# Performance work log

Hardware: AMD Instinct MI355X
Metric: run time of the kernel (lower is better)

## Reference

```python
import jax, jax.numpy as jnp
import numpy as np

HIDDEN = 1024

def setup_inputs() -> dict:
    key = jax.random.key(0)
    ks = jax.random.split(key, 7)
    B, S, H = 4, 2048, HIDDEN
    scale = 1.0 / np.sqrt(H)
    x = jax.random.normal(ks[0], (B, S, H), dtype=jnp.float32)
    Wq = jax.random.normal(ks[1], (H, H), dtype=jnp.float32) * scale
    Wk = jax.random.normal(ks[2], (H, H), dtype=jnp.float32) * scale
    Wv = jax.random.normal(ks[3], (H, H), dtype=jnp.float32) * scale
    bq = jax.random.normal(ks[4], (H,), dtype=jnp.float32) * 0.01
    bk = jax.random.normal(ks[5], (H,), dtype=jnp.float32) * 0.01
    bv = jax.random.normal(ks[6], (H,), dtype=jnp.float32) * 0.01
    return {"x": x, "Wq": Wq, "bq": bq, "Wk": Wk, "bk": bk, "Wv": Wv, "bv": bv}

def reference(x, Wq, bq, Wk, bk, Wv, bv):
    H = x.shape[-1]
    # Linear layers: y = x @ W^T + b (torch convention)
    Q = jnp.einsum('bsh,oh->bso', x, Wq) + bq
    K = jnp.einsum('bsh,oh->bso', x, Wk) + bk
    V = jnp.einsum('bsh,oh->bso', x, Wv) + bv
    # full O(S^2) score matrix, scaled by sqrt(hidden_dim) as in the source
    scores = jnp.einsum('bqh,bkh->bqk', Q, K) / jnp.sqrt(jnp.asarray(H, x.dtype))
    weights = jax.nn.softmax(scores, axis=-1)  # dropout is identity at inference
    out = jnp.einsum('bqk,bkh->bqh', weights, V)
    return out
```

## Files before the change

kernel.cpp:

```cpp
#include <hip/hip_runtime.h>
#include <hip/hip_bf16.h>

typedef __attribute__((ext_vector_type(8))) short bf16x8;
typedef __attribute__((ext_vector_type(4))) float f32x4;
typedef unsigned short u16;
typedef unsigned int u32;


__device__ __forceinline__ u16 f2bf(float f) {
  union { float f; u32 u; } v; v.f = f;
  u32 r = v.u + 0x7FFFu + ((v.u >> 16) & 1u);
  return (u16)(r >> 16);
}

__device__ __forceinline__ void gload_lds16(const u16* g, u16* l) {
  __builtin_amdgcn_global_load_lds(
      (const __attribute__((address_space(1))) u32*)(const void*)g,
      (__attribute__((address_space(3))) u32*)(void*)l, 16, 0, 0);
}


__global__ __launch_bounds__(256) void cvt_all(const float* __restrict__ x,
                                               const float* __restrict__ wq,
                                               const float* __restrict__ wk,
                                               const float* __restrict__ wv,
                                               u16* __restrict__ xb,
                                               u16* __restrict__ wcat) {
  const int bid = blockIdx.x;
  const float* src; u16* dst; size_t base;
  if (bid < 4096) { src = x; dst = xb; base = (size_t)bid * 2048; }
  else {
    int w = bid - 4096, s = w >> 9;
    src = (s == 0) ? wq : ((s == 1) ? wk : wv);
    dst = wcat + (size_t)s * 1048576;
    base = (size_t)(w & 511) * 2048;
  }
  size_t i = base + (size_t)threadIdx.x * 8;
  const float4* p = (const float4*)(src + i);
  float4 a = p[0], b = p[1];
  union { u16 u[8]; uint4 v; } r;
  r.u[0] = f2bf(a.x); r.u[1] = f2bf(a.y); r.u[2] = f2bf(a.z); r.u[3] = f2bf(a.w);
  r.u[4] = f2bf(b.x); r.u[5] = f2bf(b.y); r.u[6] = f2bf(b.z); r.u[7] = f2bf(b.w);
  *(uint4*)(dst + i) = r.v;
}


template<int MODE, int BM, int BN>
__global__ __launch_bounds__(512, 2) void gemm_pipe(
    const u16* __restrict__ A, const u16* __restrict__ B,
    const float* __restrict__ b0, const float* __restrict__ b1,
    const float* __restrict__ b2,
    void* __restrict__ o0, void* __restrict__ o1, void* __restrict__ o2,
    float* __restrict__ lsum, int lda, int ldb, int nkt,
    long Abat, long Bbat) {
  extern __shared__ u16 lds[];
  constexpr int NMT = BM / 32;
  constexpr int ANL = BM / 64;
  constexpr int BNL = BN / 64;
  constexpr int ASZ = BM * 64, BSZ = BN * 64;

  const int tid = threadIdx.x;
  const int lane = tid & 63, wv = tid >> 6;
  const int lr = lane & 15, lg = lane >> 4;
  const int wm = wv >> 2, wn = wv & 3;
  const int bm = blockIdx.x * BM, bn = blockIdx.y * BN;
  const int bz = blockIdx.z;

  const u16* Ab; const u16* Bb;
  if constexpr (MODE == 3) {
    Ab = A;
    Bb = B + (size_t)Bbat * (bm >> 11);
  } else {
    Ab = A + (size_t)Abat * bz;
    Bb = B + (size_t)Bbat * bz;
  }

  f32x4 acc[NMT][4];
#pragma unroll
  for (int i = 0; i < NMT; ++i)
#pragma unroll
    for (int j = 0; j < 4; ++j) acc[i][j] = (f32x4)0.0f;

  auto stage = [&](int kt, int buf) {
    u16* As = lds + buf * (ASZ + BSZ);
    u16* Bs = As + ASZ;
    const int k0 = kt * 64;
#pragma unroll
    for (int j = 0; j < ANL; ++j) {
      int id = j * 512 + tid, row = id >> 3, c = id & 7, cg = c ^ (row & 7);
      gload_lds16(Ab + (size_t)(bm + row) * lda + k0 + cg * 8, As + id * 8);
    }
#pragma unroll
    for (int j = 0; j < BNL; ++j) {
      int id = j * 512 + tid, row = id >> 3, c = id & 7, cg = c ^ (row & 7);
      gload_lds16(Bb + (size_t)(bn + row) * ldb + k0 + cg * 8, Bs + id * 8);
    }
  };

  stage(0, 0);
  __syncthreads();

  for (int kt = 0; kt < nkt; ++kt) {
    if (kt + 1 < nkt) stage(kt + 1, (kt + 1) & 1);
    __builtin_amdgcn_sched_barrier(0);
    const u16* As = lds + (kt & 1) * (ASZ + BSZ);
    const u16* Bs = As + ASZ;
#pragma unroll
    for (int kk = 0; kk < 2; ++kk) {
      bf16x8 a[NMT], b[4];
#pragma unroll
      for (int mt = 0; mt < NMT; ++mt) {
        int row = wm * (BM / 2) + mt * 16 + lr;
        int kc = (kk * 4 + lg) ^ (row & 7);
        a[mt] = *(const bf16x8*)(As + row * 64 + kc * 8);
      }
#pragma unroll
      for (int nt = 0; nt < 4; ++nt) {
        int row = wn * 64 + nt * 16 + lr;
        int kc = (kk * 4 + lg) ^ (row & 7);
        b[nt] = *(const bf16x8*)(Bs + row * 64 + kc * 8);
      }
#pragma unroll
      for (int mt = 0; mt < NMT; ++mt)
#pragma unroll
        for (int nt = 0; nt < 4; ++nt)
          acc[mt][nt] = __builtin_amdgcn_mfma_f32_16x16x32_bf16(a[mt], b[nt], acc[mt][nt], 0, 0, 0);
    }
    __syncthreads();
  }

  if constexpr (MODE == 0) {
    const int sel = bn >> 10;
    const float* bp = (sel == 0) ? b0 : ((sel == 1) ? b1 : b2);
#pragma unroll
    for (int nt = 0; nt < 4; ++nt) {
      int gcol = bn + wn * 64 + nt * 16 + lr;
      int col = gcol & 1023;
      float bv = bp[col];
#pragma unroll
      for (int mt = 0; mt < NMT; ++mt) {
        int grow0 = bm + wm * (BM / 2) + mt * 16 + lg * 4;
        if (sel < 2) {
          u16* o = sel ? (u16*)o1 : (u16*)o0;
#pragma unroll
          for (int r = 0; r < 4; ++r)
            o[(size_t)(grow0 + r) * 1024 + col] = f2bf(acc[mt][nt][r] + bv);
        } else {
          u16* o = (u16*)o2;
          int batch = grow0 >> 11, s = grow0 & 2047;
          union { u16 u[4]; uint2 v; } pk;
#pragma unroll
          for (int r = 0; r < 4; ++r) pk.u[r] = f2bf(acc[mt][nt][r] + bv);
          *(uint2*)(o + (((size_t)(batch * 1024 + col)) << 11) + s) = pk.v;
        }
      }
    }
  } else if constexpr (MODE == 2) {
    u16* P = (u16*)o0 + (size_t)2048 * 2048 * bz;
    float psum[NMT][4];
#pragma unroll
    for (int mt = 0; mt < NMT; ++mt)
#pragma unroll
      for (int r = 0; r < 4; ++r) psum[mt][r] = 0.0f;
#pragma unroll
    for (int nt = 0; nt < 4; ++nt) {
      int gcol = bn + wn * 64 + nt * 16 + lr;
#pragma unroll
      for (int mt = 0; mt < NMT; ++mt) {
        int grow0 = bm + wm * (BM / 2) + mt * 16 + lg * 4;
#pragma unroll
        for (int r = 0; r < 4; ++r) {
          float e = __expf(acc[mt][nt][r] * 0.03125f);
          P[(size_t)(grow0 + r) * 2048 + gcol] = f2bf(e);
          psum[mt][r] += e;
        }
      }
    }
#pragma unroll
    for (int mt = 0; mt < NMT; ++mt)
#pragma unroll
      for (int r = 0; r < 4; ++r) {
#pragma unroll
        for (int off = 1; off < 16; off <<= 1)
          psum[mt][r] += __shfl_xor(psum[mt][r], off);
      }
    if (lr == 0) {
#pragma unroll
      for (int mt = 0; mt < NMT; ++mt) {
        int grow0 = bm + wm * (BM / 2) + mt * 16 + lg * 4;
#pragma unroll
        for (int r = 0; r < 4; ++r)
          atomicAdd(&lsum[bz * 2048 + grow0 + r], psum[mt][r]);
      }
    }
  } else {
    float* o = (float*)o0;
#pragma unroll
    for (int mt = 0; mt < NMT; ++mt) {
      int grow0 = bm + wm * (BM / 2) + mt * 16 + lg * 4;
      float inv[4];
#pragma unroll
      for (int r = 0; r < 4; ++r) inv[r] = 1.0f / lsum[grow0 + r];
#pragma unroll
      for (int nt = 0; nt < 4; ++nt) {
        int gcol = bn + wn * 64 + nt * 16 + lr;
#pragma unroll
        for (int r = 0; r < 4; ++r)
          o[(size_t)(grow0 + r) * 1024 + gcol] = acc[mt][nt][r] * inv[r];
      }
    }
  }
}


extern "C" void kernel_launch(void* const* d_in, const int* in_sizes, int n_in,
                              void* d_out, int out_size, void* d_ws, size_t ws_size,
                              hipStream_t stream) {
  const float* x  = (const float*)d_in[0];
  const float* Wq = (const float*)d_in[1];
  const float* bq = (const float*)d_in[2];
  const float* Wk = (const float*)d_in[3];
  const float* bk = (const float*)d_in[4];
  const float* Wv = (const float*)d_in[5];
  const float* bv = (const float*)d_in[6];
  float* out = (float*)d_out;

  char* ws = (char*)d_ws;
  u16*   xb   = (u16*)  (ws + ((size_t)0  << 20));
  u16*   wcat = (u16*)  (ws + ((size_t)16 << 20));
  float* lvec = (float*)(ws + ((size_t)23 << 20));
  u16*   qb   = (u16*)  (ws + ((size_t)24 << 20));
  u16*   kb   = (u16*)  (ws + ((size_t)40 << 20));
  u16*   vtb  = (u16*)  (ws + ((size_t)56 << 20));
  u16*   Pb   = (u16*)  (ws + ((size_t)72 << 20));

  hipFuncSetAttribute((const void*)&gemm_pipe<0, 256, 256>,
                      hipFuncAttributeMaxDynamicSharedMemorySize, 131072);
  hipFuncSetAttribute((const void*)&gemm_pipe<2, 256, 256>,
                      hipFuncAttributeMaxDynamicSharedMemorySize, 131072);
  hipFuncSetAttribute((const void*)&gemm_pipe<3, 128, 256>,
                      hipFuncAttributeMaxDynamicSharedMemorySize, 98304);

  hipMemsetAsync(lvec, 0, 8192 * sizeof(float), stream);
  cvt_all<<<dim3(5632), dim3(256), 0, stream>>>(x, Wq, Wk, Wv, xb, wcat);

  gemm_pipe<0, 256, 256><<<dim3(32, 12, 1), dim3(512), 131072, stream>>>(
      xb, wcat, bq, bk, bv, qb, kb, vtb, nullptr, 1024, 1024, 16, 0, 0);

  gemm_pipe<2, 256, 256><<<dim3(8, 8, 4), dim3(512), 131072, stream>>>(
      qb, kb, nullptr, nullptr, nullptr, Pb, nullptr, nullptr, lvec,
      1024, 1024, 16, (long)2048 * 1024, (long)2048 * 1024);

  gemm_pipe<3, 128, 256><<<dim3(64, 4, 1), dim3(512), 98304, stream>>>(
      Pb, vtb, nullptr, nullptr, nullptr, out, nullptr, nullptr, lvec,
      2048, 2048, 32, 0, (long)1024 * 2048);
}
```

Before: 248.6 us.

## Use dedicated 128x128 QKV GEMM kernel and fold lsum zeroing into convert

Replaces the 256x256 pipelined QKV projection launch (384 blocks) with a new non-pipelined 128x128-tile kernel launched on 1536 blocks of 256 threads, which fills the CUs better on a GPU with many compute units. The memset of the row-sum vector is removed and the zeroing is done by an extra block in the conversion kernel, saving one launch. The new GEMM drops double buffering, so global-to-LDS loads are no longer overlapped with MFMA work within a block and the kernel relies on occupancy to hide that latency.

```diff
diff --git a/kernel.cpp b/kernel.cpp
--- a/kernel.cpp
+++ b/kernel.cpp
@@ -25,8 +25,16 @@
                                                const float* __restrict__ wk,
                                                const float* __restrict__ wv,
                                                u16* __restrict__ xb,
-                                               u16* __restrict__ wcat) {
+                                               u16* __restrict__ wcat,
+                                               float* __restrict__ lvec) {
   const int bid = blockIdx.x;
+  if (bid == 5632) {
+    float4 z = make_float4(0.f, 0.f, 0.f, 0.f);
+#pragma unroll
+    for (int j = 0; j < 8; ++j)
+      *(float4*)(lvec + (j * 256 + threadIdx.x) * 4) = z;
+    return;
+  }
   const float* src; u16* dst; size_t base;
   if (bid < 4096) { src = x; dst = xb; base = (size_t)bid * 2048; }
   else {
@@ -45,14 +53,91 @@
 }
 
 
+__global__ __launch_bounds__(256) void gemm_qkv(
+    const u16* __restrict__ A, const u16* __restrict__ B,
+    const float* __restrict__ b0, const float* __restrict__ b1,
+    const float* __restrict__ b2,
+    u16* __restrict__ oq, u16* __restrict__ ok, u16* __restrict__ ovt) {
+  __shared__ u16 As[8192];
+  __shared__ u16 Bs[8192];
+  const int tid = threadIdx.x;
+  const int lane = tid & 63, wv = tid >> 6;
+  const int lr = lane & 15, lg = lane >> 4;
+  const int wm = (wv >> 1) * 64, wn = (wv & 1) * 64;
+  const int bm = blockIdx.x * 128, bn = blockIdx.y * 128;
+
+  f32x4 acc[4][4];
+#pragma unroll
+  for (int i = 0; i < 4; ++i)
+#pragma unroll
+    for (int j = 0; j < 4; ++j) acc[i][j] = (f32x4)0.0f;
+
+  for (int kt = 0; kt < 16; ++kt) {
+    const int k0 = kt * 64;
+#pragma unroll
+    for (int i = 0; i < 4; ++i) {
+      int id = i * 256 + tid;
+      int row = id >> 3, c = id & 7;
+      int cg = c ^ (row & 7);
+      gload_lds16(A + (size_t)(bm + row) * 1024 + k0 + cg * 8, As + id * 8);
+      gload_lds16(B + (size_t)(bn + row) * 1024 + k0 + cg * 8, Bs + id * 8);
+    }
+    __syncthreads();
+#pragma unroll
+    for (int kk = 0; kk < 2; ++kk) {
+      bf16x8 a[4], b[4];
+#pragma unroll
+      for (int mt = 0; mt < 4; ++mt) {
+        int row = wm + mt * 16 + lr;
+        int kc = (kk * 4 + lg) ^ (row & 7);
+        a[mt] = *(const bf16x8*)(As + row * 64 + kc * 8);
+      }
+#pragma unroll
+      for (int nt = 0; nt < 4; ++nt) {
+        int row = wn + nt * 16 + lr;
+        int kc = (kk * 4 + lg) ^ (row & 7);
+        b[nt] = *(const bf16x8*)(Bs + row * 64 + kc * 8);
+      }
+#pragma unroll
+      for (int mt = 0; mt < 4; ++mt)
+#pragma unroll
+        for (int nt = 0; nt < 4; ++nt)
+          acc[mt][nt] = __builtin_amdgcn_mfma_f32_16x16x32_bf16(a[mt], b[nt], acc[mt][nt], 0, 0, 0);
+    }
+    __syncthreads();
+  }
+
+  const int sel = bn >> 10;
+  const float* bp = (sel == 0) ? b0 : ((sel == 1) ? b1 : b2);
+#pragma unroll
+  for (int nt = 0; nt < 4; ++nt) {
+    int col = (bn + wn + nt * 16 + lr) & 1023;
+    float bv = bp[col];
+#pragma unroll
+    for (int mt = 0; mt < 4; ++mt) {
+      int grow0 = bm + wm + mt * 16 + lg * 4;
+      if (sel < 2) {
+        u16* o = sel ? ok : oq;
+#pragma unroll
+        for (int r = 0; r < 4; ++r)
+          o[(size_t)(grow0 + r) * 1024 + col] = f2bf(acc[mt][nt][r] + bv);
+      } else {
+        int batch = grow0 >> 11, s = grow0 & 2047;
+        union { u16 u[4]; uint2 v; } pk;
+#pragma unroll
+        for (int r = 0; r < 4; ++r) pk.u[r] = f2bf(acc[mt][nt][r] + bv);
+        *(uint2*)(ovt + (((size_t)(batch * 1024 + col)) << 11) + s) = pk.v;
+      }
+    }
+  }
+}
+
+
 template<int MODE, int BM, int BN>
 __global__ __launch_bounds__(512, 2) void gemm_pipe(
     const u16* __restrict__ A, const u16* __restrict__ B,
-    const float* __restrict__ b0, const float* __restrict__ b1,
-    const float* __restrict__ b2,
-    void* __restrict__ o0, void* __restrict__ o1, void* __restrict__ o2,
-    float* __restrict__ lsum, int lda, int ldb, int nkt,
-    long Abat, long Bbat) {
+    void* __restrict__ o0, float* __restrict__ lsum,
+    int lda, int ldb, int nkt, long Abat, long Bbat) {
   extern __shared__ u16 lds[];
   constexpr int NMT = BM / 32;
   constexpr int ANL = BM / 64;
@@ -67,13 +152,8 @@
   const int bz = blockIdx.z;
 
   const u16* Ab; const u16* Bb;
-  if constexpr (MODE == 3) {
-    Ab = A;
-    Bb = B + (size_t)Bbat * (bm >> 11);
-  } else {
-    Ab = A + (size_t)Abat * bz;
-    Bb = B + (size_t)Bbat * bz;
-  }
+  if constexpr (MODE == 3) { Ab = A; Bb = B + (size_t)Bbat * (bm >> 11); }
+  else { Ab = A + (size_t)Abat * bz; Bb = B + (size_t)Bbat * bz; }
 
   f32x4 acc[NMT][4];
 #pragma unroll
@@ -129,33 +209,7 @@
     __syncthreads();
   }
 
-  if constexpr (MODE == 0) {
-    const int sel = bn >> 10;
-    const float* bp = (sel == 0) ? b0 : ((sel == 1) ? b1 : b2);
-#pragma unroll
-    for (int nt = 0; nt < 4; ++nt) {
-      int gcol = bn + wn * 64 + nt * 16 + lr;
-      int col = gcol & 1023;
-      float bv = bp[col];
-#pragma unroll
-      for (int mt = 0; mt < NMT; ++mt) {
-        int grow0 = bm + wm * (BM / 2) + mt * 16 + lg * 4;
-        if (sel < 2) {
-          u16* o = sel ? (u16*)o1 : (u16*)o0;
-#pragma unroll
-          for (int r = 0; r < 4; ++r)
-            o[(size_t)(grow0 + r) * 1024 + col] = f2bf(acc[mt][nt][r] + bv);
-        } else {
-          u16* o = (u16*)o2;
-          int batch = grow0 >> 11, s = grow0 & 2047;
-          union { u16 u[4]; uint2 v; } pk;
-#pragma unroll
-          for (int r = 0; r < 4; ++r) pk.u[r] = f2bf(acc[mt][nt][r] + bv);
-          *(uint2*)(o + (((size_t)(batch * 1024 + col)) << 11) + s) = pk.v;
-        }
-      }
-    }
-  } else if constexpr (MODE == 2) {
+  if constexpr (MODE == 2) {
     u16* P = (u16*)o0 + (size_t)2048 * 2048 * bz;
     float psum[NMT][4];
 #pragma unroll
@@ -234,24 +288,19 @@
   u16*   vtb  = (u16*)  (ws + ((size_t)56 << 20));
   u16*   Pb   = (u16*)  (ws + ((size_t)72 << 20));
 
-  hipFuncSetAttribute((const void*)&gemm_pipe<0, 256, 256>,
-                      hipFuncAttributeMaxDynamicSharedMemorySize, 131072);
   hipFuncSetAttribute((const void*)&gemm_pipe<2, 256, 256>,
                       hipFuncAttributeMaxDynamicSharedMemorySize, 131072);
   hipFuncSetAttribute((const void*)&gemm_pipe<3, 128, 256>,
                       hipFuncAttributeMaxDynamicSharedMemorySize, 98304);
 
-  hipMemsetAsync(lvec, 0, 8192 * sizeof(float), stream);
-  cvt_all<<<dim3(5632), dim3(256), 0, stream>>>(x, Wq, Wk, Wv, xb, wcat);
-
-  gemm_pipe<0, 256, 256><<<dim3(32, 12, 1), dim3(512), 131072, stream>>>(
-      xb, wcat, bq, bk, bv, qb, kb, vtb, nullptr, 1024, 1024, 16, 0, 0);
+  cvt_all<<<dim3(5633), dim3(256), 0, stream>>>(x, Wq, Wk, Wv, xb, wcat, lvec);
+
+  gemm_qkv<<<dim3(64, 24, 1), dim3(256), 0, stream>>>(
+      xb, wcat, bq, bk, bv, qb, kb, vtb);
 
   gemm_pipe<2, 256, 256><<<dim3(8, 8, 4), dim3(512), 131072, stream>>>(
-      qb, kb, nullptr, nullptr, nullptr, Pb, nullptr, nullptr, lvec,
-      1024, 1024, 16, (long)2048 * 1024, (long)2048 * 1024);
+      qb, kb, Pb, lvec, 1024, 1024, 16, (long)2048 * 1024, (long)2048 * 1024);
 
   gemm_pipe<3, 128, 256><<<dim3(64, 4, 1), dim3(512), 98304, stream>>>(
-      Pb, vtb, nullptr, nullptr, nullptr, out, nullptr, nullptr, lvec,
-      2048, 2048, 32, 0, (long)1024 * 2048);
-}
+      Pb, vtb, out, lvec, 2048, 2048, 32, 0, (long)1024 * 2048);
+}
```

New measurement: 246.1 us. Within noise of the previous version (-1.0%).
